# Kernel optimization log

Hardware: AMD Instinct MI355X
Metric: run time of the kernel (lower is better)

Reference implementation:

```python
import jax, jax.numpy as jnp
import numpy as np

BLOCK = 32          # MX block size along the contraction dim
E4M3_MAX = 448.0    # max finite magnitude of float8_e4m3fn
E4M3_MAX_EXP = 8.0  # floor(log2(448)) = 8


def mxfp8_quant_dequant(t):
    """Simulate MXFP8 (OCP MX spec): per-32-block E8M0 power-of-two scale,
    elements cast to float8_e4m3fn, then dequantized back to fp32."""
    orig_shape = t.shape
    tb = t.reshape(-1, BLOCK)
    amax = jnp.max(jnp.abs(tb), axis=-1, keepdims=True)
    # E8M0 shared scale: 2^(floor(log2(amax)) - emax_e4m3)
    exp = jnp.floor(jnp.log2(jnp.maximum(amax, 2.0 ** -126))) - E4M3_MAX_EXP
    scale = jnp.exp2(exp)
    q = jnp.clip(tb / scale, -E4M3_MAX, E4M3_MAX)
    q = q.astype(jnp.float8_e4m3fn).astype(t.dtype)  # round-to-nearest fp8
    return (q * scale).reshape(orig_shape)


def setup_inputs() -> dict:
    key = jax.random.key(0)
    k1, k2, k3 = jax.random.split(key, 3)
    B, S, D_IN, D_OUT = 4, 4096, 4096, 4096
    x = jax.random.normal(k1, (B, S, D_IN), dtype=jnp.float32)
    weight = jax.random.normal(k2, (D_OUT, D_IN), dtype=jnp.float32) * 0.02
    bias = jax.random.normal(k3, (D_OUT,), dtype=jnp.float32) * 0.02
    return {"x": x, "weight": weight, "bias": bias}


def reference(x, weight, bias):
    B, S, D_IN = x.shape
    # Inline activation quantization to MXFP8 (blocks of 32 along in_features)
    x2 = x.reshape(-1, D_IN)                 # [B*S, D_IN]
    x_dq = mxfp8_quant_dequant(x2)
    # Weight is stored MXFP8-quantized; dequantize with its block scales
    w_dq = mxfp8_quant_dequant(weight)       # [D_OUT, D_IN]
    out = jnp.einsum('nk,ok->no', x_dq, w_dq) + bias  # microscaled GEMM
    return out.reshape(B, S, -1)
```

## Files before the change

### kernel.cpp

```cpp
#include <hip/hip_runtime.h>
#include <hip/hip_bf16.h>
#include <stdint.h>

typedef __attribute__((ext_vector_type(8))) short bf16x8;
typedef __attribute__((ext_vector_type(4))) float f32x4;
typedef __attribute__((ext_vector_type(8))) unsigned short u16x8;

#define BM 256
#define BN 256
#define BKT 64
#define ABYTES (BM * BKT * 2)
#define BBYTES (BN * BKT * 2)
#define BUFBYTES (ABYTES + BBYTES)

__device__ __forceinline__ float mx_qd_elem(float x, int e) {
    float xs = ldexpf(x, -e);
    xs = fminf(448.f, fmaxf(-448.f, xs));
    float a = fabsf(xs);
    float r;
    if (a < 0.015625f) {
        r = ldexpf(rintf(ldexpf(a, 9)), -9);
    } else {
        int E = (int)((__float_as_uint(a) >> 23) & 0xFF) - 127;
        r = ldexpf(rintf(ldexpf(a, 3 - E)), E - 3);
    }
    r = copysignf(r, xs);
    return ldexpf(r, e);
}

__global__ __launch_bounds__(256) void mx_quant_bf16(
    const float* __restrict__ in, uint16_t* __restrict__ out, int nblk) {
    int t = blockIdx.x * 256 + threadIdx.x;
    if (t >= nblk) return;
    const float4* p = (const float4*)(in + (size_t)t * 32);
    float v[32];
#pragma unroll
    for (int i = 0; i < 8; ++i) {
        float4 fv = p[i];
        v[4 * i + 0] = fv.x; v[4 * i + 1] = fv.y;
        v[4 * i + 2] = fv.z; v[4 * i + 3] = fv.w;
    }
    float amax = 0.f;
#pragma unroll
    for (int i = 0; i < 32; ++i) amax = fmaxf(amax, fabsf(v[i]));
    amax = fmaxf(amax, 1.17549435e-38f);
    int e = (int)((__float_as_uint(amax) >> 23) & 0xFF) - 127 - 8;

    unsigned short res[32];
#pragma unroll
    for (int i = 0; i < 32; ++i) {
        float d = mx_qd_elem(v[i], e);
        res[i] = (unsigned short)(__float_as_uint(d) >> 16);
    }
    u16x8* o = (u16x8*)(out + (size_t)t * 32);
#pragma unroll
    for (int j = 0; j < 4; ++j) {
        u16x8 pack;
#pragma unroll
        for (int i = 0; i < 8; ++i) pack[i] = res[8 * j + i];
        o[j] = pack;
    }
}

#define GLOAD(srcp, ldsoff)                                                     \
    __builtin_amdgcn_global_load_lds(                                           \
        (const __attribute__((address_space(1))) void*)(srcp),                  \
        (__attribute__((address_space(3))) void*)&lds[ldsoff], 16, 0, 0)

__global__ __launch_bounds__(512, 2) void gemm_ck_bf16(
    const uint16_t* __restrict__ A, const uint16_t* __restrict__ B,
    const float* __restrict__ bias, float* __restrict__ C,
    int Nrows, int K, int O) {
    __shared__ __align__(16) uint8_t lds[2 * BUFBYTES];

    const int tid  = threadIdx.x;
    const int lane = tid & 63;
    const int w    = tid >> 6;
    const int f    = lane & 15, g = lane >> 4;
    const int wm   = w >> 2,    wn = w & 3;

    const int nwg  = gridDim.x * gridDim.y;
    const int flat = blockIdx.y * gridDim.x + blockIdx.x;
    const int swz  = (flat & 7) * (nwg >> 3) + (flat >> 3);
    const int bx   = swz % gridDim.x, by = swz / gridDim.x;
    const int rowBase = by * BM, colBase = bx * BN;

    const int sri = tid >> 3;
    const int ssc = ((tid & 7) * 16) ^ ((sri & 7) << 4);
    const int sld = tid * 16;
    const size_t K2 = (size_t)K * 2;
    const uint8_t* gAr[4]; const uint8_t* gBr[4];
#pragma unroll
    for (int r = 0; r < 4; ++r) {
        gAr[r] = (const uint8_t*)A + (size_t)(rowBase + r * 64 + sri) * K2 + ssc;
        gBr[r] = (const uint8_t*)B + (size_t)(colBase + r * 64 + sri) * K2 + ssc;
    }
#define STAGE(t) do {                                                           \
        const int _buf = ((t) & 1) * BUFBYTES;                                  \
        const size_t _kb = (size_t)(t) * (BKT * 2);                             \
        _Pragma("unroll")                                                       \
        for (int _i = 0; _i < 4; ++_i)                                          \
            GLOAD(gAr[_i] + _kb, _buf + _i * 8192 + sld);                       \
        _Pragma("unroll")                                                       \
        for (int _i = 0; _i < 4; ++_i)                                          \
            GLOAD(gBr[_i] + _kb, _buf + ABYTES + _i * 8192 + sld);              \
    } while (0)

    int aoff[8][2], boff[4][2];
#pragma unroll
    for (int kk = 0; kk < 2; ++kk) {
        const int colb = (kk * 64 + g * 16) ^ ((f & 7) << 4);
#pragma unroll
        for (int m = 0; m < 8; ++m)
            aoff[m][kk] = (wm * 128 + m * 16 + f) * 128 + colb;
#pragma unroll
        for (int n = 0; n < 4; ++n)
            boff[n][kk] = ABYTES + (wn * 64 + n * 16 + f) * 128 + colb;
    }

    f32x4 acc[8][4];
#pragma unroll
    for (int m = 0; m < 8; ++m)
#pragma unroll
        for (int n = 0; n < 4; ++n)
#pragma unroll
            for (int j = 0; j < 4; ++j) acc[m][n][j] = 0.f;

    const int nt = K / BKT;

#define WAITL(N) do {                                                           \
        asm volatile("s_waitcnt lgkmcnt(" #N ")" ::: "memory");                 \
        __builtin_amdgcn_sched_barrier(0);                                      \
    } while (0)
#define MFMA_C(MB, AF, BF) do {                                                 \
        __builtin_amdgcn_s_setprio(1);                                          \
        _Pragma("unroll") for (int _m = 0; _m < 4; ++_m)                        \
        _Pragma("unroll") for (int _n = 0; _n < 4; ++_n)                        \
            acc[(MB) + _m][_n] = __builtin_amdgcn_mfma_f32_16x16x32_bf16(       \
                AF[_m], BF[_n], acc[(MB) + _m][_n], 0, 0, 0);                   \
        __builtin_amdgcn_s_setprio(0);                                          \
    } while (0)

    STAGE(0);
    asm volatile("s_waitcnt vmcnt(0)" ::: "memory");
    __builtin_amdgcn_sched_barrier(0);
    __builtin_amdgcn_s_barrier();
    __builtin_amdgcn_sched_barrier(0);

    for (int t = 0; t < nt; ++t) {
        const int bb = (t & 1) * BUFBYTES;
        const bool pf = (t + 1) < nt;
        bf16x8 bA[4], bB[4], aLo[4], aHi[4], aLo1[4], aHi1[4];

#pragma unroll
        for (int n = 0; n < 4; ++n) bA[n] = *(const bf16x8*)&lds[bb + boff[n][0]];
#pragma unroll
        for (int m = 0; m < 4; ++m) aLo[m] = *(const bf16x8*)&lds[bb + aoff[m][0]];
#pragma unroll
        for (int m = 0; m < 4; ++m) aHi[m] = *(const bf16x8*)&lds[bb + aoff[4 + m][0]];
        if (pf) STAGE(t + 1);
        WAITL(4);
        MFMA_C(0, aLo, bA);
#pragma unroll
        for (int n = 0; n < 4; ++n) bB[n] = *(const bf16x8*)&lds[bb + boff[n][1]];
#pragma unroll
        for (int m = 0; m < 4; ++m) aLo1[m] = *(const bf16x8*)&lds[bb + aoff[m][1]];
        WAITL(8);
        MFMA_C(4, aHi, bA);
#pragma unroll
        for (int m = 0; m < 4; ++m) aHi1[m] = *(const bf16x8*)&lds[bb + aoff[4 + m][1]];
        WAITL(4);
        MFMA_C(0, aLo1, bB);
        WAITL(0);
        MFMA_C(4, aHi1, bB);
        asm volatile("s_waitcnt vmcnt(0)" ::: "memory");
        __builtin_amdgcn_sched_barrier(0);
        __builtin_amdgcn_s_barrier();
        __builtin_amdgcn_sched_barrier(0);
    }
#undef STAGE
#undef WAITL
#undef MFMA_C

    const int qr = g * 4;
#pragma unroll
    for (int n = 0; n < 4; ++n) {
        int col = colBase + wn * 64 + n * 16 + f;
        float bv = bias[col];
#pragma unroll
        for (int m = 0; m < 8; ++m) {
            int r0 = rowBase + wm * 128 + m * 16 + qr;
#pragma unroll
            for (int j = 0; j < 4; ++j)
                C[(size_t)(r0 + j) * O + col] = acc[m][n][j] + bv;
        }
    }
}

extern "C" void kernel_launch(void* const* d_in, const int* in_sizes, int n_in,
                              void* d_out, int out_size, void* d_ws, size_t ws_size,
                              hipStream_t stream) {
    const float* x    = (const float*)d_in[0];
    const float* wgt  = (const float*)d_in[1];
    const float* bias = (const float*)d_in[2];
    float* out = (float*)d_out;

    const int D_OUT = in_sizes[2];
    const int D_IN  = in_sizes[1] / D_OUT;
    const int NROWS = in_sizes[0] / D_IN;

    uint16_t* xq = (uint16_t*)d_ws;
    uint16_t* wq = xq + (size_t)NROWS * D_IN;

    int nblkx = NROWS * (D_IN / 32);
    int nblkw = D_OUT * (D_IN / 32);
    mx_quant_bf16<<<dim3((nblkx + 255) / 256), dim3(256), 0, stream>>>(x, xq, nblkx);
    mx_quant_bf16<<<dim3((nblkw + 255) / 256), dim3(256), 0, stream>>>(wgt, wq, nblkw);

    dim3 grid(D_OUT / BN, NROWS / BM);
    gemm_ck_bf16<<<grid, dim3(512), 0, stream>>>(xq, wq, bias, out,
                                                 NROWS, D_IN, D_OUT);
}
```

Before: 587.3 us.

## Deepen GEMM pipeline to four LDS buffers with BK=32 and prefetch distance two

Halves the K tile to 32 and uses four LDS stages, prefetching two tiles ahead with a partial vmcnt wait so global loads have more time in flight. The LDS swizzle and fragment offsets are rewritten for the 64-byte row layout. The cost is a barrier every 32 K instead of every 64, doubling synchronisation count and giving fewer MFMAs per barrier. Total LDS usage stays the same.

After: 630.5 us. 7.3% more time.

```diff
diff --git a/kernel.cpp b/kernel.cpp
--- a/kernel.cpp
+++ b/kernel.cpp
@@ -8,10 +8,11 @@
 
 #define BM 256
 #define BN 256
-#define BKT 64
+#define BKT 32
 #define ABYTES (BM * BKT * 2)
 #define BBYTES (BN * BKT * 2)
 #define BUFBYTES (ABYTES + BBYTES)
+#define NBUF 4
 
 __device__ __forceinline__ float mx_qd_elem(float x, int e) {
     float xs = ldexpf(x, -e);
@@ -67,11 +68,11 @@
         (const __attribute__((address_space(1))) void*)(srcp),                  \
         (__attribute__((address_space(3))) void*)&lds[ldsoff], 16, 0, 0)
 
-__global__ __launch_bounds__(512, 2) void gemm_ck_bf16(
+__global__ __launch_bounds__(512, 2) void gemm_d2_bf16(
     const uint16_t* __restrict__ A, const uint16_t* __restrict__ B,
     const float* __restrict__ bias, float* __restrict__ C,
     int Nrows, int K, int O) {
-    __shared__ __align__(16) uint8_t lds[2 * BUFBYTES];
+    __shared__ __align__(16) uint8_t lds[NBUF * BUFBYTES];
 
     const int tid  = threadIdx.x;
     const int lane = tid & 63;
@@ -85,37 +86,33 @@
     const int bx   = swz % gridDim.x, by = swz / gridDim.x;
     const int rowBase = by * BM, colBase = bx * BN;
 
-    const int sri = tid >> 3;
-    const int ssc = ((tid & 7) * 16) ^ ((sri & 7) << 4);
+    const int srow = tid >> 2;
+    const int ssc  = ((tid & 3) ^ ((srow >> 1) & 3)) * 16;
+    const size_t K2 = (size_t)K * 2;
+    const uint8_t* gA0 = (const uint8_t*)A + (size_t)(rowBase + srow) * K2 + ssc;
+    const uint8_t* gA1 = (const uint8_t*)A + (size_t)(rowBase + 128 + srow) * K2 + ssc;
+    const uint8_t* gB0 = (const uint8_t*)B + (size_t)(colBase + srow) * K2 + ssc;
+    const uint8_t* gB1 = (const uint8_t*)B + (size_t)(colBase + 128 + srow) * K2 + ssc;
     const int sld = tid * 16;
-    const size_t K2 = (size_t)K * 2;
-    const uint8_t* gAr[4]; const uint8_t* gBr[4];
-#pragma unroll
-    for (int r = 0; r < 4; ++r) {
-        gAr[r] = (const uint8_t*)A + (size_t)(rowBase + r * 64 + sri) * K2 + ssc;
-        gBr[r] = (const uint8_t*)B + (size_t)(colBase + r * 64 + sri) * K2 + ssc;
-    }
 #define STAGE(t) do {                                                           \
-        const int _buf = ((t) & 1) * BUFBYTES;                                  \
+        const int _buf = ((t) & 3) * BUFBYTES;                                  \
         const size_t _kb = (size_t)(t) * (BKT * 2);                             \
-        _Pragma("unroll")                                                       \
-        for (int _i = 0; _i < 4; ++_i)                                          \
-            GLOAD(gAr[_i] + _kb, _buf + _i * 8192 + sld);                       \
-        _Pragma("unroll")                                                       \
-        for (int _i = 0; _i < 4; ++_i)                                          \
-            GLOAD(gBr[_i] + _kb, _buf + ABYTES + _i * 8192 + sld);              \
+        GLOAD(gA0 + _kb, _buf + sld);                                           \
+        GLOAD(gA1 + _kb, _buf + 8192 + sld);                                    \
+        GLOAD(gB0 + _kb, _buf + ABYTES + sld);                                  \
+        GLOAD(gB1 + _kb, _buf + ABYTES + 8192 + sld);                           \
     } while (0)
 
-    int aoff[8][2], boff[4][2];
-#pragma unroll
-    for (int kk = 0; kk < 2; ++kk) {
-        const int colb = (kk * 64 + g * 16) ^ ((f & 7) << 4);
-#pragma unroll
-        for (int m = 0; m < 8; ++m)
-            aoff[m][kk] = (wm * 128 + m * 16 + f) * 128 + colb;
-#pragma unroll
-        for (int n = 0; n < 4; ++n)
-            boff[n][kk] = ABYTES + (wn * 64 + n * 16 + f) * 128 + colb;
+    int aoff[8], boff[4];
+#pragma unroll
+    for (int m = 0; m < 8; ++m) {
+        int r = wm * 128 + m * 16 + f;
+        aoff[m] = r * 64 + ((g ^ ((r >> 1) & 3)) * 16);
+    }
+#pragma unroll
+    for (int n = 0; n < 4; ++n) {
+        int r = wn * 64 + n * 16 + f;
+        boff[n] = ABYTES + r * 64 + ((g ^ ((r >> 1) & 3)) * 16);
     }
 
     f32x4 acc[8][4];
@@ -142,38 +139,30 @@
     } while (0)
 
     STAGE(0);
-    asm volatile("s_waitcnt vmcnt(0)" ::: "memory");
+    STAGE(1);
+    asm volatile("s_waitcnt vmcnt(4)" ::: "memory");
     __builtin_amdgcn_sched_barrier(0);
     __builtin_amdgcn_s_barrier();
     __builtin_amdgcn_sched_barrier(0);
 
     for (int t = 0; t < nt; ++t) {
-        const int bb = (t & 1) * BUFBYTES;
-        const bool pf = (t + 1) < nt;
-        bf16x8 bA[4], bB[4], aLo[4], aHi[4], aLo1[4], aHi1[4];
-
-#pragma unroll
-        for (int n = 0; n < 4; ++n) bA[n] = *(const bf16x8*)&lds[bb + boff[n][0]];
-#pragma unroll
-        for (int m = 0; m < 4; ++m) aLo[m] = *(const bf16x8*)&lds[bb + aoff[m][0]];
-#pragma unroll
-        for (int m = 0; m < 4; ++m) aHi[m] = *(const bf16x8*)&lds[bb + aoff[4 + m][0]];
-        if (pf) STAGE(t + 1);
+        const int bb = (t & 3) * BUFBYTES;
+        const bool pf = (t + 2) < nt;
+        bf16x8 bA[4], aLo[4], aHi[4];
+
+#pragma unroll
+        for (int n = 0; n < 4; ++n) bA[n] = *(const bf16x8*)&lds[bb + boff[n]];
+#pragma unroll
+        for (int m = 0; m < 4; ++m) aLo[m] = *(const bf16x8*)&lds[bb + aoff[m]];
+#pragma unroll
+        for (int m = 0; m < 4; ++m) aHi[m] = *(const bf16x8*)&lds[bb + aoff[4 + m]];
+        if (pf) STAGE(t + 2);
         WAITL(4);
         MFMA_C(0, aLo, bA);
-#pragma unroll
-        for (int n = 0; n < 4; ++n) bB[n] = *(const bf16x8*)&lds[bb + boff[n][1]];
-#pragma unroll
-        for (int m = 0; m < 4; ++m) aLo1[m] = *(const bf16x8*)&lds[bb + aoff[m][1]];
-        WAITL(8);
+        WAITL(0);
         MFMA_C(4, aHi, bA);
-#pragma unroll
-        for (int m = 0; m < 4; ++m) aHi1[m] = *(const bf16x8*)&lds[bb + aoff[4 + m][1]];
-        WAITL(4);
-        MFMA_C(0, aLo1, bB);
-        WAITL(0);
-        MFMA_C(4, aHi1, bB);
-        asm volatile("s_waitcnt vmcnt(0)" ::: "memory");
+        if (pf) asm volatile("s_waitcnt vmcnt(4)" ::: "memory");
+        else    asm volatile("s_waitcnt vmcnt(0)" ::: "memory");
         __builtin_amdgcn_sched_barrier(0);
         __builtin_amdgcn_s_barrier();
         __builtin_amdgcn_sched_barrier(0);
@@ -218,6 +207,6 @@
     mx_quant_bf16<<<dim3((nblkw + 255) / 256), dim3(256), 0, stream>>>(wgt, wq, nblkw);
 
     dim3 grid(D_OUT / BN, NROWS / BM);
-    gemm_ck_bf16<<<grid, dim3(512), 0, stream>>>(xq, wq, bias, out,
+    gemm_d2_bf16<<<grid, dim3(512), 0, stream>>>(xq, wq, bias, out,
                                                  NROWS, D_IN, D_OUT);
 }
```
